# Optimization experiments

Measured on AMD Instinct MI355X. Metric: run time of the kernel, lower is better.

Reference implementation:

```python
import jax, jax.numpy as jnp
import numpy as np

D_IN = 2048
D_OUT = 2048
NUM_HEADS = 16
HEAD_DIM = D_OUT // NUM_HEADS


def setup_inputs() -> dict:
    key = jax.random.key(0)
    k_x, k_qkv, k_proj, k_b = jax.random.split(key, 4)
    x = jax.random.normal(k_x, (2, 2048, D_IN), dtype=jnp.float32)
    # torch Linear(d_in, 3*d_out, bias=False): weight [3*d_out, d_in]; store transposed [d_in, 3*d_out]
    Wqkv = jax.random.normal(k_qkv, (D_IN, 3 * D_OUT), dtype=jnp.float32) / np.sqrt(D_IN)
    Wproj = jax.random.normal(k_proj, (D_OUT, D_OUT), dtype=jnp.float32) / np.sqrt(D_OUT)
    bproj = jax.random.normal(k_b, (D_OUT,), dtype=jnp.float32) * 0.01
    return {"x": x, "Wqkv": Wqkv, "Wproj": Wproj, "bproj": bproj}


def reference(x, Wqkv, Wproj, bproj):
    B, S, _ = x.shape
    qkv = x @ Wqkv  # [B, S, 3*D_OUT]
    qkv = qkv.reshape(B, S, 3, NUM_HEADS, HEAD_DIM)
    qkv = jnp.transpose(qkv, (2, 0, 3, 1, 4))  # [3, B, H, S, Dh]
    q, k, v = qkv[0], qkv[1], qkv[2]
    scale = 1.0 / np.sqrt(HEAD_DIM).astype(np.float32)
    scores = jnp.einsum('bhqd,bhkd->bhqk', q, k) * scale  # [B, H, S, S]
    causal = jnp.tril(jnp.ones((S, S), dtype=bool))
    scores = jnp.where(causal, scores, jnp.finfo(scores.dtype).min)
    attn = jax.nn.softmax(scores, axis=-1)
    out = jnp.einsum('bhqk,bhkd->bhqd', attn, v)  # [B, H, S, Dh]
    out = jnp.transpose(out, (0, 2, 1, 3)).reshape(B, S, D_OUT)
    return out @ Wproj + bproj
```

## Files before the change

kernel.cpp:

```cpp
#include <hip/hip_runtime.h>
#include <stdint.h>

typedef __attribute__((ext_vector_type(8))) short short8;
typedef __attribute__((ext_vector_type(4))) float f32x4;
typedef __attribute__((ext_vector_type(16))) float f32x16;
typedef __attribute__((ext_vector_type(4))) unsigned short u16x4;

typedef unsigned short u16;

constexpr int S_LEN = 2048;
constexpr int DH    = 128;

__device__ __forceinline__ u16 f2bf(float f) {
    union { float f; unsigned u; } v; v.f = f;
    unsigned r = v.u + 0x7FFFu + ((v.u >> 16) & 1u);
    return (u16)(r >> 16);
}
__device__ __forceinline__ void gl_lds16(const void* g, void* l) {
    __builtin_amdgcn_global_load_lds((const __attribute__((address_space(1))) void*)g,
                                     (__attribute__((address_space(3))) void*)l,
                                     16, 0, 0);
}

__global__ __launch_bounds__(256) void convx(const float* __restrict__ src,
                                             u16* __restrict__ dst) {
    size_t i = ((size_t)blockIdx.x * 256 + threadIdx.x) * 8;
    f32x4 a = *(const f32x4*)(src + i);
    f32x4 b = *(const f32x4*)(src + i + 4);
    short8 r;
    r[0] = (short)f2bf(a[0]); r[1] = (short)f2bf(a[1]);
    r[2] = (short)f2bf(a[2]); r[3] = (short)f2bf(a[3]);
    r[4] = (short)f2bf(b[0]); r[5] = (short)f2bf(b[1]);
    r[6] = (short)f2bf(b[2]); r[7] = (short)f2bf(b[3]);
    *(short8*)(dst + i) = r;
}

__global__ void convT(const float* __restrict__ src, u16* __restrict__ dst,
                      int rows, int cols) {
    __shared__ u16 tile[32][33];
    int c0 = blockIdx.x * 32, r0 = blockIdx.y * 32;
    int tx = threadIdx.x, ty = threadIdx.y;
#pragma unroll
    for (int i = 0; i < 32; i += 8)
        tile[ty + i][tx] = f2bf(src[(size_t)(r0 + ty + i) * cols + c0 + tx]);
    __syncthreads();
#pragma unroll
    for (int i = 0; i < 32; i += 8)
        dst[(size_t)(c0 + ty + i) * rows + r0 + tx] = tile[tx][ty + i];
}

__global__ __launch_bounds__(512, 2) void gemm_qkv(
        const u16* __restrict__ A, const u16* __restrict__ BT,
        u16* __restrict__ Qo, u16* __restrict__ Ko, u16* __restrict__ VTo) {
    __shared__ __align__(16) u16 lA[2][128 * 64];
    __shared__ __align__(16) u16 lB[2][256 * 64];
    const int tid = threadIdx.x;
    const int lane = tid & 63, wave = tid >> 6;
    const int quad = lane >> 4, l16 = lane & 15;
    const int wr = wave >> 2, wc = wave & 3;
    const int m0 = blockIdx.y * 128, n0 = blockIdx.x * 256;
    const int sw = l16 & 7;
    const int c4 = tid & 7;
    f32x4 acc[4][4] = {};

    auto stageA = [&](int t1, int nb) {
#pragma unroll
        for (int j = 0; j < 2; ++j) {
            int idx = j * 512 + tid;
            int row = idx >> 3;
            gl_lds16(A + (size_t)(m0 + row) * 2048 + t1 * 64 + ((c4 ^ (row & 7)) * 8),
                     &lA[nb][row * 64 + c4 * 8]);
        }
    };
    auto stageB = [&](int h, int t1, int nb) {
#pragma unroll
        for (int j = 0; j < 2; ++j) {
            int rih = (j * 512 + tid) >> 3;
            int row = (rih & 31) + h * 32 + (rih >> 5) * 64;
            gl_lds16(BT + (size_t)(n0 + row) * 2048 + t1 * 64 + ((c4 ^ (row & 7)) * 8),
                     &lB[nb][row * 64 + c4 * 8]);
        }
    };

    stageA(0, 0); stageB(0, 0, 0); stageB(1, 0, 0);

    constexpr int NT = 32;
    for (int t = 0; t < NT; ++t) {
        const int buf = t & 1, nb = buf ^ 1;
        const bool pf = (t + 1 < NT);
        asm volatile("s_waitcnt vmcnt(2)\n\ts_barrier" ::: "memory");
        short8 af[4][2], bf0[2][2];
        const int abase = (wr * 64 + l16) * 64;
        const int bbase = (wc * 64 + l16) * 64;
#pragma unroll
        for (int m = 0; m < 4; ++m)
#pragma unroll
            for (int ks = 0; ks < 2; ++ks)
                af[m][ks] = *(const short8*)&lA[buf][abase + m * 1024 + (((ks * 4 + quad) ^ sw)) * 8];
#pragma unroll
        for (int n = 0; n < 2; ++n)
#pragma unroll
            for (int ks = 0; ks < 2; ++ks)
                bf0[n][ks] = *(const short8*)&lB[buf][bbase + n * 1024 + (((ks * 4 + quad) ^ sw)) * 8];
        if (pf) { stageA(t + 1, nb); stageB(0, t + 1, nb); }
        __builtin_amdgcn_s_setprio(1);
#pragma unroll
        for (int m = 0; m < 4; ++m)
#pragma unroll
            for (int n = 0; n < 2; ++n)
#pragma unroll
                for (int ks = 0; ks < 2; ++ks)
                    acc[m][n] = __builtin_amdgcn_mfma_f32_16x16x32_bf16(
                        af[m][ks], bf0[n][ks], acc[m][n], 0, 0, 0);
        __builtin_amdgcn_s_setprio(0);
        if (pf) asm volatile("s_waitcnt vmcnt(4)\n\ts_barrier" ::: "memory");
        else    asm volatile("s_waitcnt vmcnt(0)\n\ts_barrier" ::: "memory");
        short8 bf1[2][2];
#pragma unroll
        for (int n = 0; n < 2; ++n)
#pragma unroll
            for (int ks = 0; ks < 2; ++ks)
                bf1[n][ks] = *(const short8*)&lB[buf][bbase + 2048 + n * 1024 + (((ks * 4 + quad) ^ sw)) * 8];
        if (pf) stageB(1, t + 1, nb);
        __builtin_amdgcn_s_setprio(1);
#pragma unroll
        for (int m = 0; m < 4; ++m)
#pragma unroll
            for (int n = 0; n < 2; ++n)
#pragma unroll
                for (int ks = 0; ks < 2; ++ks)
                    acc[m][n + 2] = __builtin_amdgcn_mfma_f32_16x16x32_bf16(
                        af[m][ks], bf1[n][ks], acc[m][n + 2], 0, 0, 0);
        __builtin_amdgcn_s_setprio(0);
    }

#pragma unroll
    for (int m = 0; m < 4; ++m) {
        int r0r = m0 + wr * 64 + m * 16 + quad * 4;
        int b = r0r >> 11, s0 = r0r & 2047;
#pragma unroll
        for (int n = 0; n < 4; ++n) {
            int cc = n0 + wc * 64 + n * 16 + l16;
            int which = cc >> 11, hd = (cc >> 7) & 15, dh = cc & 127;
            if (which < 2) {
                u16* dst = which == 0 ? Qo : Ko;
#pragma unroll
                for (int rg = 0; rg < 4; ++rg)
                    dst[(size_t)((b * 16 + hd) * 2048 + s0 + rg) * 128 + dh] = f2bf(acc[m][n][rg]);
            } else {
                u16x4 v;
#pragma unroll
                for (int rg = 0; rg < 4; ++rg) v[rg] = f2bf(acc[m][n][rg]);
                *(u16x4*)&VTo[((size_t)(b * 16 + hd) * 128 + dh) * 2048 + s0] = v;
            }
        }
    }
}

__global__ __launch_bounds__(256, 2) void attn_kern(
        u16* __restrict__ QOp, const u16* __restrict__ Kp,
        const u16* __restrict__ VTp) {
    __shared__ __align__(16) u16 lK[2][64 * 128];
    __shared__ __align__(16) u16 lV[2][128 * 64];
    const int tid = threadIdx.x, lane = tid & 63, wave = tid >> 6;
    const int ql = lane & 31, hi = lane >> 5;
    const int qb = (blockIdx.y < 8) ? (15 - (int)blockIdx.y) : ((int)blockIdx.y - 8);
    const int bh = blockIdx.x;
    const int qbase = qb * 128 + wave * 32;
    const int qmax = qbase + 31;
    const int nkt = 2 * qb + 2;
    u16* Qh = QOp + (size_t)bh * S_LEN * DH;
    const u16* Kh = Kp + (size_t)bh * S_LEN * DH;
    const u16* VTh = VTp + (size_t)bh * DH * S_LEN;

    short8 qf[8];
#pragma unroll
    for (int c = 0; c < 8; ++c)
        qf[c] = *(const short8*)&Qh[(size_t)(qbase + ql) * 128 + c * 16 + hi * 8];

    f32x16 acc[4] = {};
    float mrun = -1e30f, lrun = 0.f;
    const float SC = 0.08838834764831845f * 1.44269504088896f;

    auto stage = [&](int kt, int b) {
        const u16* ks = Kh + (size_t)kt * 64 * 128;
#pragma unroll
        for (int p = 0; p < 4; ++p) {
            int slot = p * 256 + tid;
            int row = slot >> 4, c4 = slot & 15;
            gl_lds16(ks + row * 128 + ((c4 ^ (row & 15)) * 8), &lK[b][slot * 8]);
        }
        const u16* vs = VTh + kt * 64;
#pragma unroll
        for (int p = 0; p < 4; ++p) {
            int slot = p * 256 + tid;
            int row = slot >> 3, c4 = slot & 7;
            gl_lds16(vs + (size_t)row * 2048 + ((c4 ^ (row & 7)) * 8), &lV[b][slot * 8]);
        }
    };

    stage(0, 0);
    __syncthreads();

    for (int kt = 0; kt < nkt; ++kt) {
        const int buf = kt & 1;
        if (kt + 1 < nkt) stage(kt + 1, buf ^ 1);
        if (kt * 64 <= qmax) {
            const bool part = (kt * 64 + 63 > qbase);
            f32x16 s0 = {}, s1 = {};
            __builtin_amdgcn_s_setprio(1);
#pragma unroll
            for (int c = 0; c < 8; ++c) {
                int sl = ((c * 2 + hi) ^ (ql & 15)) * 8;
                short8 k0 = *(const short8*)&lK[buf][ql * 128 + sl];
                short8 k1 = *(const short8*)&lK[buf][(32 + ql) * 128 + sl];
                s0 = __builtin_amdgcn_mfma_f32_32x32x16_bf16(k0, qf[c], s0, 0, 0, 0);
                s1 = __builtin_amdgcn_mfma_f32_32x32x16_bf16(k1, qf[c], s1, 0, 0, 0);
            }
            __builtin_amdgcn_s_setprio(0);
            float pv0[16], pv1[16];
            float pm = -1e30f;
            const int qg = qbase + ql;
#pragma unroll
            for (int r = 0; r < 16; ++r) {
                int krow = (r & 3) + 8 * (r >> 2) + 4 * hi;
                float a = s0[r] * SC;
                float b = s1[r] * SC;
                if (part) {
                    if (kt * 64 + krow > qg)      a = -1e30f;
                    if (kt * 64 + 32 + krow > qg) b = -1e30f;
                }
                pv0[r] = a; pv1[r] = b;
                pm = fmaxf(pm, fmaxf(a, b));
            }
            pm = fmaxf(pm, __shfl_xor(pm, 32));
            if (__any(pm - mrun > 8.f)) {
                float mn = fmaxf(mrun, pm);
                float al = exp2f(mrun - mn);
                mrun = mn;
                lrun *= al;
#pragma unroll
                for (int r = 0; r < 16; ++r) {
                    float ar = __shfl(al, (r & 3) + 8 * (r >> 2) + 4 * hi);
#pragma unroll
                    for (int dc = 0; dc < 4; ++dc)
                        acc[dc][r] *= ar;
                }
            }
            float rs = 0.f;
#pragma unroll
            for (int r = 0; r < 16; ++r) {
                pv0[r] = exp2f(pv0[r] - mrun);
                pv1[r] = exp2f(pv1[r] - mrun);
                rs += pv0[r] + pv1[r];
            }
            rs += __shfl_xor(rs, 32);
            lrun += rs;
            unsigned X0[8], X1[8];
#pragma unroll
            for (int i = 0; i < 8; ++i) {
                X0[i] = (unsigned)f2bf(pv0[2 * i]) | ((unsigned)f2bf(pv0[2 * i + 1]) << 16);
                X1[i] = (unsigned)f2bf(pv1[2 * i]) | ((unsigned)f2bf(pv1[2 * i + 1]) << 16);
            }
            short8 pa[4];
#pragma unroll
            for (int t = 0; t < 2; ++t)
#pragma unroll
                for (int h = 0; h < 2; ++h) {
                    unsigned x0 = t ? X1[4 * h + 0] : X0[4 * h + 0];
                    unsigned x1 = t ? X1[4 * h + 1] : X0[4 * h + 1];
                    unsigned x2 = t ? X1[4 * h + 2] : X0[4 * h + 2];
                    unsigned x3 = t ? X1[4 * h + 3] : X0[4 * h + 3];
                    unsigned sx0 = (unsigned)__shfl_xor((int)x0, 32);
                    unsigned sx1 = (unsigned)__shfl_xor((int)x1, 32);
                    unsigned sx2 = (unsigned)__shfl_xor((int)x2, 32);
                    unsigned sx3 = (unsigned)__shfl_xor((int)x3, 32);
                    union { unsigned u[4]; short8 s; } uf;
                    uf.u[0] = hi ? sx2 : x0;
                    uf.u[1] = hi ? sx3 : x1;
                    uf.u[2] = hi ? x2 : sx0;
                    uf.u[3] = hi ? x3 : sx1;
                    pa[t * 2 + h] = uf.s;
                }
            __builtin_amdgcn_s_setprio(1);
#pragma unroll
            for (int dc = 0; dc < 4; ++dc) {
                const int rv = dc * 32 + ql;
#pragma unroll
                for (int kc = 0; kc < 4; ++kc) {
                    short8 vf = *(const short8*)&lV[buf][rv * 64 + (((kc * 2 + hi) ^ (ql & 7)) * 8)];
                    acc[dc] = __builtin_amdgcn_mfma_f32_32x32x16_bf16(pa[kc], vf, acc[dc], 0, 0, 0);
                }
            }
            __builtin_amdgcn_s_setprio(0);
        }
        __syncthreads();
    }

    float linv = 1.f / lrun;
#pragma unroll
    for (int r = 0; r < 16; ++r) {
        int qr = (r & 3) + 8 * (r >> 2) + 4 * hi;
        float lr = __shfl(linv, qr);
        int qq = qbase + qr;
#pragma unroll
        for (int dc = 0; dc < 4; ++dc)
            Qh[(size_t)qq * 128 + dc * 32 + ql] = f2bf(acc[dc][r] * lr);
    }
}

__global__ __launch_bounds__(256, 2) void gemm_proj(
        const u16* __restrict__ QO, const u16* __restrict__ BT,
        const float* __restrict__ bias, float* __restrict__ out) {
    __shared__ __align__(16) u16 lA[2][128 * 64];
    __shared__ __align__(16) u16 lB[2][128 * 64];
    const int tid = threadIdx.x;
    const int lane = tid & 63, wave = tid >> 6;
    const int quad = lane >> 4, l16 = lane & 15;
    const int wm = wave >> 1, wn = wave & 1;
    const int bid = blockIdx.x;
    const int swz = (bid & 7) * 64 + (bid >> 3);
    const int m0 = (swz >> 4) * 128, n0 = (swz & 15) * 128;
    const int sw = l16 & 7;
    const int c4 = tid & 7;
    f32x4 acc[4][4] = {};

    auto stageA = [&](int t1, int nb) {
#pragma unroll
        for (int j = 0; j < 4; ++j) {
            int row = (j * 256 + tid) >> 3;
            int r = m0 + row;
            int b = r >> 11, s = r & 2047;
            int k = t1 * 64 + ((c4 ^ (row & 7)) * 8);
            int h = k >> 7, dh = k & 127;
            gl_lds16(QO + ((size_t)(b * 16 + h) * 2048 + s) * 128 + dh,
                     &lA[nb][row * 64 + c4 * 8]);
        }
    };
    auto stageB = [&](int h, int t1, int nb) {
#pragma unroll
        for (int j = 0; j < 2; ++j) {
            int rih = (j * 256 + tid) >> 3;
            int row = (rih & 31) + h * 32 + (rih >> 5) * 64;
            gl_lds16(BT + (size_t)(n0 + row) * 2048 + t1 * 64 + ((c4 ^ (row & 7)) * 8),
                     &lB[nb][row * 64 + c4 * 8]);
        }
    };

    stageB(0, 0, 0);
    asm volatile("" ::: "memory");
    stageA(0, 0);
    asm volatile("" ::: "memory");
    stageB(1, 0, 0);

    constexpr int NT = 32;
    for (int t = 0; t < NT; ++t) {
        const int buf = t & 1, nb = buf ^ 1;
        const bool pf = (t + 1 < NT);
        asm volatile("s_waitcnt vmcnt(2)\n\ts_barrier" ::: "memory");
        short8 af[4][2], bf0[2][2];
        const int abase = (wm * 64 + l16) * 64;
        const int bbase = (wn * 64 + l16) * 64;
#pragma unroll
        for (int m = 0; m < 4; ++m)
#pragma unroll
            for (int ks = 0; ks < 2; ++ks)
                af[m][ks] = *(const short8*)&lA[buf][abase + m * 1024 + (((ks * 4 + quad) ^ sw)) * 8];
#pragma unroll
        for (int n = 0; n < 2; ++n)
#pragma unroll
            for (int ks = 0; ks < 2; ++ks)
                bf0[n][ks] = *(const short8*)&lB[buf][bbase + n * 1024 + (((ks * 4 + quad) ^ sw)) * 8];
        if (pf) {
            stageB(0, t + 1, nb);
            asm volatile("" ::: "memory");
            stageA(t + 1, nb);
        }
        __builtin_amdgcn_s_setprio(1);
#pragma unroll
        for (int m = 0; m < 4; ++m)
#pragma unroll
            for (int n = 0; n < 2; ++n)
#pragma unroll
                for (int ks = 0; ks < 2; ++ks)
                    acc[m][n] = __builtin_amdgcn_mfma_f32_16x16x32_bf16(
                        af[m][ks], bf0[n][ks], acc[m][n], 0, 0, 0);
        __builtin_amdgcn_s_setprio(0);
        if (pf) asm volatile("s_waitcnt vmcnt(6)\n\ts_barrier" ::: "memory");
        else    asm volatile("s_waitcnt vmcnt(0)\n\ts_barrier" ::: "memory");
        short8 bf1[2][2];
#pragma unroll
        for (int n = 0; n < 2; ++n)
#pragma unroll
            for (int ks = 0; ks < 2; ++ks)
                bf1[n][ks] = *(const short8*)&lB[buf][bbase + 2048 + n * 1024 + (((ks * 4 + quad) ^ sw)) * 8];
        if (pf) stageB(1, t + 1, nb);
        __builtin_amdgcn_s_setprio(1);
#pragma unroll
        for (int m = 0; m < 4; ++m)
#pragma unroll
            for (int n = 0; n < 2; ++n)
#pragma unroll
                for (int ks = 0; ks < 2; ++ks)
                    acc[m][n + 2] = __builtin_amdgcn_mfma_f32_16x16x32_bf16(
                        af[m][ks], bf1[n][ks], acc[m][n + 2], 0, 0, 0);
        __builtin_amdgcn_s_setprio(0);
    }

#pragma unroll
    for (int m = 0; m < 4; ++m) {
        int r0r = m0 + wm * 64 + m * 16 + quad * 4;
#pragma unroll
        for (int n = 0; n < 4; ++n) {
            int cc = n0 + wn * 64 + n * 16 + l16;
            float bv = bias[cc];
#pragma unroll
            for (int rg = 0; rg < 4; ++rg)
                out[(size_t)(r0r + rg) * 2048 + cc] = acc[m][n][rg] + bv;
        }
    }
}

extern "C" void kernel_launch(void* const* d_in, const int* in_sizes, int n_in,
                              void* d_out, int out_size, void* d_ws, size_t ws_size,
                              hipStream_t stream) {
    const float *x = nullptr, *Wqkv = nullptr, *Wproj = nullptr, *bproj = nullptr;
    for (int i = 0; i < n_in; ++i) {
        int sz = in_sizes[i];
        if      (sz == 2 * 2048 * 2048) x     = (const float*)d_in[i];
        else if (sz == 2048 * 6144)     Wqkv  = (const float*)d_in[i];
        else if (sz == 2048 * 2048)     Wproj = (const float*)d_in[i];
        else if (sz == 2048)            bproj = (const float*)d_in[i];
    }
    float* out = (float*)d_out;

    u16* xb     = (u16*)d_ws;
    u16* WqkvT  = xb    + (size_t)4096 * 2048;
    u16* Qb     = WqkvT + (size_t)6144 * 2048;
    u16* Kb     = Qb    + (size_t)32 * 2048 * 128;
    u16* VTb    = Kb    + (size_t)32 * 2048 * 128;
    u16* WprojT = xb;

    convx<<<dim3(4096), dim3(256), 0, stream>>>(x, xb);
    convT<<<dim3(192, 64), dim3(32, 8), 0, stream>>>(Wqkv, WqkvT, 2048, 6144);
    gemm_qkv<<<dim3(24, 32), dim3(512), 0, stream>>>(xb, WqkvT, Qb, Kb, VTb);
    convT<<<dim3(64, 64), dim3(32, 8), 0, stream>>>(Wproj, WprojT, 2048, 2048);
    attn_kern<<<dim3(32, 16), dim3(256), 0, stream>>>(Qb, Kb, VTb);
    gemm_proj<<<dim3(512), dim3(256), 0, stream>>>(Qb, WprojT, bproj, out);
}
```

Before: 367.5 us.

## Split K/V staging with fine-grained vmcnt waits and vectorize transpose conversion

The attention loop now stages K and V tiles separately. K for the next tile is issued after the QK MFMAs, and V after the PV MFMAs, with s_waitcnt vmcnt barriers so each wait covers only the data about to be used. This aims to overlap global-to-LDS loads with softmax and MFMA work instead of one full sync per tile. The weight transpose-to-bf16 kernel is rewritten to use 64x64 tiles with float4 loads and 4-wide bf16 stores to cut memory instructions. The cost is an extra barrier per iteration and reliance on exact vmcnt counting.

```diff
diff --git a/kernel.cpp b/kernel.cpp
--- a/kernel.cpp
+++ b/kernel.cpp
@@ -35,18 +35,34 @@
     *(short8*)(dst + i) = r;
 }
 
-__global__ void convT(const float* __restrict__ src, u16* __restrict__ dst,
-                      int rows, int cols) {
-    __shared__ u16 tile[32][33];
-    int c0 = blockIdx.x * 32, r0 = blockIdx.y * 32;
-    int tx = threadIdx.x, ty = threadIdx.y;
-#pragma unroll
-    for (int i = 0; i < 32; i += 8)
-        tile[ty + i][tx] = f2bf(src[(size_t)(r0 + ty + i) * cols + c0 + tx]);
+__global__ __launch_bounds__(256) void convT(const float* __restrict__ src,
+                                             u16* __restrict__ dst,
+                                             int rows, int cols) {
+    __shared__ u16 t[64][65];
+    const int c0 = blockIdx.x * 64, r0 = blockIdx.y * 64;
+    const int tid = threadIdx.x;
+    const int colq = (tid & 15) * 4;
+    const int rw   = tid >> 4;
+#pragma unroll
+    for (int p = 0; p < 4; ++p) {
+        int row = p * 16 + rw;
+        f32x4 v = *(const f32x4*)(src + (size_t)(r0 + row) * cols + c0 + colq);
+        t[colq + 0][row] = f2bf(v[0]);
+        t[colq + 1][row] = f2bf(v[1]);
+        t[colq + 2][row] = f2bf(v[2]);
+        t[colq + 3][row] = f2bf(v[3]);
+    }
     __syncthreads();
-#pragma unroll
-    for (int i = 0; i < 32; i += 8)
-        dst[(size_t)(c0 + ty + i) * rows + r0 + tx] = tile[tx][ty + i];
+    const int rowq = (tid & 15) * 4;
+    const int cw   = tid >> 4;
+#pragma unroll
+    for (int p = 0; p < 4; ++p) {
+        int col = p * 16 + cw;
+        u16x4 o;
+        o[0] = t[col][rowq + 0]; o[1] = t[col][rowq + 1];
+        o[2] = t[col][rowq + 2]; o[3] = t[col][rowq + 3];
+        *(u16x4*)(dst + (size_t)(c0 + col) * rows + r0 + rowq) = o;
+    }
 }
 
 __global__ __launch_bounds__(512, 2) void gemm_qkv(
@@ -182,7 +198,7 @@
     float mrun = -1e30f, lrun = 0.f;
     const float SC = 0.08838834764831845f * 1.44269504088896f;
 
-    auto stage = [&](int kt, int b) {
+    auto stageK = [&](int kt, int b) {
         const u16* ks = Kh + (size_t)kt * 64 * 128;
 #pragma unroll
         for (int p = 0; p < 4; ++p) {
@@ -190,6 +206,8 @@
             int row = slot >> 4, c4 = slot & 15;
             gl_lds16(ks + row * 128 + ((c4 ^ (row & 15)) * 8), &lK[b][slot * 8]);
         }
+    };
+    auto stageV = [&](int kt, int b) {
         const u16* vs = VTh + kt * 64;
 #pragma unroll
         for (int p = 0; p < 4; ++p) {
@@ -199,13 +217,16 @@
         }
     };
 
-    stage(0, 0);
-    __syncthreads();
+    stageK(0, 0);
+    stageV(0, 0);
+    asm volatile("s_waitcnt vmcnt(4)\n\ts_barrier" ::: "memory");
 
     for (int kt = 0; kt < nkt; ++kt) {
         const int buf = kt & 1;
-        if (kt + 1 < nkt) stage(kt + 1, buf ^ 1);
-        if (kt * 64 <= qmax) {
+        const bool more = kt + 1 < nkt;
+        const bool compute = (kt * 64 <= qmax);
+        float pv0[16], pv1[16];
+        if (compute) {
             const bool part = (kt * 64 + 63 > qbase);
             f32x16 s0 = {}, s1 = {};
             __builtin_amdgcn_s_setprio(1);
@@ -218,7 +239,7 @@
                 s1 = __builtin_amdgcn_mfma_f32_32x32x16_bf16(k1, qf[c], s1, 0, 0, 0);
             }
             __builtin_amdgcn_s_setprio(0);
-            float pv0[16], pv1[16];
+            if (more) stageK(kt + 1, buf ^ 1);
             float pm = -1e30f;
             const int qg = qbase + ql;
 #pragma unroll
@@ -256,6 +277,12 @@
             }
             rs += __shfl_xor(rs, 32);
             lrun += rs;
+        } else if (more) {
+            stageK(kt + 1, buf ^ 1);
+        }
+        if (more) asm volatile("s_waitcnt vmcnt(4)\n\ts_barrier" ::: "memory");
+        else      asm volatile("s_waitcnt vmcnt(0)\n\ts_barrier" ::: "memory");
+        if (compute) {
             unsigned X0[8], X1[8];
 #pragma unroll
             for (int i = 0; i < 8; ++i) {
@@ -294,7 +321,10 @@
             }
             __builtin_amdgcn_s_setprio(0);
         }
-        __syncthreads();
+        if (more) {
+            stageV(kt + 1, buf ^ 1);
+            asm volatile("s_waitcnt vmcnt(4)\n\ts_barrier" ::: "memory");
+        }
     }
 
     float linv = 1.f / lrun;
@@ -442,9 +472,9 @@
     u16* WprojT = xb;
 
     convx<<<dim3(4096), dim3(256), 0, stream>>>(x, xb);
-    convT<<<dim3(192, 64), dim3(32, 8), 0, stream>>>(Wqkv, WqkvT, 2048, 6144);
+    convT<<<dim3(96, 32), dim3(256), 0, stream>>>(Wqkv, WqkvT, 2048, 6144);
     gemm_qkv<<<dim3(24, 32), dim3(512), 0, stream>>>(xb, WqkvT, Qb, Kb, VTb);
-    convT<<<dim3(64, 64), dim3(32, 8), 0, stream>>>(Wproj, WprojT, 2048, 2048);
+    convT<<<dim3(32, 32), dim3(256), 0, stream>>>(Wproj, WprojT, 2048, 2048);
     attn_kern<<<dim3(32, 16), dim3(256), 0, stream>>>(Qb, Kb, VTb);
     gemm_proj<<<dim3(512), dim3(256), 0, stream>>>(Qb, WprojT, bproj, out);
 }
```

After: 371.3 us. About the same (+1.0%).
